# Performance work log

Measured on AMD Instinct MI355X. Metric: run time of the kernel, lower is better.

Reference implementation:

```python
import jax, jax.numpy as jnp
import numpy as np

EMBED_DIM = 768
NUM_HEADS = 12
HEAD_DIM = EMBED_DIM // NUM_HEADS


def setup_inputs() -> dict:
    key = jax.random.key(0)
    ks = jax.random.split(key, 9)
    B, N, D = 1, 4096, EMBED_DIM
    s = 1.0 / np.sqrt(D)
    x = jax.random.normal(ks[0], (B, N, D), dtype=jnp.float32)
    Wq = jax.random.normal(ks[1], (D, D), dtype=jnp.float32) * s
    Wk = jax.random.normal(ks[2], (D, D), dtype=jnp.float32) * s
    Wv = jax.random.normal(ks[3], (D, D), dtype=jnp.float32) * s
    Wo = jax.random.normal(ks[4], (D, D), dtype=jnp.float32) * s
    bq = jax.random.normal(ks[5], (D,), dtype=jnp.float32) * 0.01
    bk = jax.random.normal(ks[6], (D,), dtype=jnp.float32) * 0.01
    bv = jax.random.normal(ks[7], (D,), dtype=jnp.float32) * 0.01
    bo = jax.random.normal(ks[8], (D,), dtype=jnp.float32) * 0.01
    return {"x": x, "Wq": Wq, "bq": bq, "Wk": Wk, "bk": bk,
            "Wv": Wv, "bv": bv, "Wo": Wo, "bo": bo}


def reference(x, Wq, bq, Wk, bk, Wv, bv, Wo, bo):
    B, N, D = x.shape
    h, d = NUM_HEADS, HEAD_DIM
    # projections; torch Linear computes x @ W.T + b, here W is stored as (in, out)
    q = (x @ Wq + bq).reshape(B, N, h, d).transpose(0, 2, 1, 3)  # [B,h,N,d]
    k = (x @ Wk + bk).reshape(B, N, h, d).transpose(0, 2, 1, 3)
    v = (x @ Wv + bv).reshape(B, N, h, d).transpose(0, 2, 1, 3)
    scores = jnp.einsum('bhnd,bhmd->bhnm', q, k) / np.sqrt(d)  # [B,h,N,N]
    attn = jax.nn.softmax(scores, axis=-1)
    out = jnp.einsum('bhnm,bhmd->bhnd', attn, v)  # [B,h,N,d]
    out = out.transpose(0, 2, 1, 3).reshape(B, N, D)
    return out @ Wo + bo
```

## Files before the change

### kernel.cpp

```cpp
#include <hip/hip_runtime.h>
#include <stdint.h>

#define EMBED 768
#define NTOK 4096
#define NHEAD 12
#define HD 64

typedef __attribute__((ext_vector_type(8))) short bf16x8;
typedef __attribute__((ext_vector_type(4))) float f32x4;
typedef __attribute__((ext_vector_type(16))) float f32x16;
typedef unsigned short ushort_t;

#define QSCALE 0.18033688011112042f

__device__ __forceinline__ unsigned short f2bf(float f) {
  union { float f; unsigned u; } c; c.f = f;
  unsigned u = c.u;
  u += 0x7fffu + ((u >> 16) & 1u);
  return (unsigned short)(u >> 16);
}

__device__ __forceinline__ void gld16(const void* g, void* l) {
  __builtin_amdgcn_global_load_lds((const __attribute__((address_space(1))) void*)g,
                                   (__attribute__((address_space(3))) void*)l,
                                   16, 0, 0);
}

__global__ void cvt_x_kernel(const float* __restrict__ x, ushort_t* __restrict__ xb) {
  size_t i = ((size_t)blockIdx.x * 256 + threadIdx.x) * 8;
  float4 a = *(const float4*)(x + i);
  float4 b = *(const float4*)(x + i + 4);
  uint4 p;
  p.x = (unsigned)f2bf(a.x) | ((unsigned)f2bf(a.y) << 16);
  p.y = (unsigned)f2bf(a.z) | ((unsigned)f2bf(a.w) << 16);
  p.z = (unsigned)f2bf(b.x) | ((unsigned)f2bf(b.y) << 16);
  p.w = (unsigned)f2bf(b.z) | ((unsigned)f2bf(b.w) << 16);
  *(uint4*)(xb + i) = p;
}

__global__ void transpose_w4_kernel(const float* __restrict__ w0, const float* __restrict__ w1,
                                    const float* __restrict__ w2, const float* __restrict__ w3,
                                    ushort_t* __restrict__ d0, ushort_t* __restrict__ d1,
                                    ushort_t* __restrict__ d2, ushort_t* __restrict__ d3) {
  __shared__ float t[32][33];
  int z = blockIdx.z;
  const float* w = (z == 0) ? w0 : (z == 1) ? w1 : (z == 2) ? w2 : w3;
  ushort_t* wt   = (z == 0) ? d0 : (z == 1) ? d1 : (z == 2) ? d2 : d3;
  int bx = blockIdx.x * 32, by = blockIdx.y * 32;
  int tx = threadIdx.x, ty = threadIdx.y;
  #pragma unroll
  for (int i = 0; i < 32; i += 8)
    t[ty + i][tx] = w[(size_t)(by + ty + i) * EMBED + bx + tx];
  __syncthreads();
  #pragma unroll
  for (int i = 0; i < 32; i += 8)
    wt[(size_t)(bx + ty + i) * EMBED + by + tx] = f2bf(t[tx][ty + i]);
}

template<int MODE>
__global__ __launch_bounds__(256)
void gemm_bt_kernel(const ushort_t* __restrict__ A, const ushort_t* __restrict__ Bt,
                    const float* __restrict__ b0, const float* __restrict__ b1,
                    const float* __restrict__ b2,
                    ushort_t* __restrict__ qo, ushort_t* __restrict__ ko,
                    ushort_t* __restrict__ vto, float* __restrict__ out) {
  __shared__ ushort_t As[128 * 32];
  __shared__ ushort_t Bs[128 * 32];
  const int K = EMBED;
  int tid = threadIdx.x, lane = tid & 63, wid = tid >> 6;
  int wy = wid >> 1, wx = wid & 1;
  int r0 = lane >> 4, cq = lane & 15;
  int brow = blockIdx.y * 128, bcol = blockIdx.x * 128;

  f32x4 acc[4][4] = {};

  for (int k0 = 0; k0 < K; k0 += 32) {
    #pragma unroll
    for (int c = 0; c < 2; ++c) {
      int chunk = wid * 2 + c;
      int eoff = chunk * 512;
      int le = eoff + lane * 8;
      int row = le >> 5, col = le & 31;
      gld16(A + (size_t)(brow + row) * K + k0 + col, As + eoff);
      gld16(Bt + (size_t)(bcol + row) * K + k0 + col, Bs + eoff);
    }
    __syncthreads();
    bf16x8 af[4], bfr[4];
    #pragma unroll
    for (int i = 0; i < 4; ++i)
      af[i] = *(const bf16x8*)(As + (wy * 64 + i * 16 + cq) * 32 + r0 * 8);
    #pragma unroll
    for (int i = 0; i < 4; ++i)
      bfr[i] = *(const bf16x8*)(Bs + (wx * 64 + i * 16 + cq) * 32 + r0 * 8);
    #pragma unroll
    for (int i = 0; i < 4; ++i)
      #pragma unroll
      for (int j = 0; j < 4; ++j)
        acc[i][j] = __builtin_amdgcn_mfma_f32_16x16x32_bf16(af[i], bfr[j], acc[i][j], 0, 0, 0);
    __syncthreads();
  }

  int sec = bcol / 768;
  int ncol0 = bcol - sec * 768;
  const float* bias = (sec == 0) ? b0 : (sec == 1) ? b1 : b2;
  #pragma unroll
  for (int i = 0; i < 4; ++i) {
    #pragma unroll
    for (int j = 0; j < 4; ++j) {
      #pragma unroll
      for (int jj = 0; jj < 4; ++jj) {
        int m = brow + wy * 64 + i * 16 + r0 * 4 + jj;
        int nn = ncol0 + wx * 64 + j * 16 + cq;
        float val = acc[i][j][jj] + bias[nn];
        if constexpr (MODE == 0) {
          int head = nn >> 6, dd = nn & 63;
          if (sec == 0)       qo[((size_t)head * NTOK + m) * HD + dd] = f2bf(val * QSCALE);
          else if (sec == 1)  ko[((size_t)head * NTOK + m) * HD + dd] = f2bf(val);
          else                vto[((size_t)head * HD + dd) * NTOK + m] = f2bf(val);
        } else {
          out[(size_t)m * EMBED + nn] = val;
        }
      }
    }
  }
}

__device__ __forceinline__ void stage32(const ushort_t* kh, const ushort_t* vh,
                                        int kb, char* buf, int lane) {
  const int srow = lane >> 3, l7 = lane & 7;
  const int ksl = l7 ^ srow;
  const ushort_t* kg = kh + (size_t)kb * HD;
  #pragma unroll
  for (int i = 0; i < 4; ++i)
    gld16(kg + ((i * 8 + srow) * HD + ksl * 8), buf + i * 1024);
  char* vbuf = buf + 4096;
  const int srw = lane >> 2;
  const int vsl = (lane & 3) ^ (srw & 3);
  const ushort_t* vg = vh + kb;
  #pragma unroll
  for (int i = 0; i < 4; ++i)
    gld16(vg + ((size_t)(i * 16 + srw) * NTOK + vsl * 8), vbuf + i * 1024);
}

__global__ __launch_bounds__(256, 2)
void flash_kernel(const ushort_t* __restrict__ q, const ushort_t* __restrict__ k,
                  const ushort_t* __restrict__ vt, ushort_t* __restrict__ o) {
  __shared__ __align__(16) char lds[65536];
  const int tid = threadIdx.x;
  const int lane = tid & 63;
  const int ks = tid >> 6;
  const int head = blockIdx.y;
  const int qbase = blockIdx.x * 64;
  const int c31 = lane & 31;
  const int hi = lane >> 5;

  const ushort_t* qh = q + (size_t)head * NTOK * HD;
  const ushort_t* kh = k + (size_t)head * NTOK * HD;
  const ushort_t* vh = vt + (size_t)head * HD * NTOK;

  char* mybase = lds + ks * 16384;

  bf16x8 qf[2][4];
  #pragma unroll
  for (int qt = 0; qt < 2; ++qt)
    #pragma unroll
    for (int dc = 0; dc < 4; ++dc)
      qf[qt][dc] = *(const bf16x8*)(qh + (size_t)(qbase + qt * 32 + c31) * HD + dc * 16 + hi * 8);

  f32x16 oacc[2][2] = {};
  float lsum[2] = {0.f, 0.f};

  stage32(kh, vh, ks * 32, mybase, lane);

  #pragma unroll 2
  for (int it = 0; it < 32; ++it) {
    const int cur = it & 1;
    if (it < 31) {
      stage32(kh, vh, (ks + 4 * (it + 1)) * 32, mybase + (cur ^ 1) * 8192, lane);
      asm volatile("s_waitcnt vmcnt(8)" ::: "memory");
    } else {
      asm volatile("s_waitcnt vmcnt(0)" ::: "memory");
    }
    const char* kbuf = mybase + cur * 8192;
    const char* vbuf = kbuf + 4096;

    f32x16 s[2] = {};
    __builtin_amdgcn_s_setprio(1);
    #pragma unroll
    for (int dc = 0; dc < 4; ++dc) {
      bf16x8 kf = *(const bf16x8*)(kbuf + c31 * 128 + (((dc * 2 + hi) ^ (c31 & 7)) * 16));
      #pragma unroll
      for (int qt = 0; qt < 2; ++qt)
        s[qt] = __builtin_amdgcn_mfma_f32_32x32x16_bf16(kf, qf[qt][dc], s[qt], 0, 0, 0);
    }
    __builtin_amdgcn_s_setprio(0);

    union pfu { unsigned u[4]; bf16x8 v; };
    pfu pf[2][2];
    #pragma unroll
    for (int qt = 0; qt < 2; ++qt) {
      float p[16];
      #pragma unroll
      for (int r = 0; r < 16; ++r)
        p[r] = __builtin_amdgcn_exp2f(s[qt][r]);
      float s4[4];
      #pragma unroll
      for (int g = 0; g < 4; ++g)
        s4[g] = (p[4 * g] + p[4 * g + 1]) + (p[4 * g + 2] + p[4 * g + 3]);
      lsum[qt] += (s4[0] + s4[1]) + (s4[2] + s4[3]);
      unsigned w[8];
      #pragma unroll
      for (int m = 0; m < 8; ++m)
        asm("v_cvt_pk_bf16_f32 %0, %1, %2" : "=v"(w[m]) : "v"(p[2 * m]), "v"(p[2 * m + 1]));
      #pragma unroll
      for (int kc = 0; kc < 2; ++kc) {
        #pragma unroll
        for (int e = 0; e < 2; ++e) {
          unsigned a = w[e + 4 * kc];
          unsigned b = w[e + 4 * kc + 2];
          asm("v_permlane32_swap_b32 %0, %1" : "+v"(a), "+v"(b));
          pf[qt][kc].u[e] = a;
          pf[qt][kc].u[e + 2] = b;
        }
      }
    }

    __builtin_amdgcn_s_setprio(1);
    #pragma unroll
    for (int kc = 0; kc < 2; ++kc)
      #pragma unroll
      for (int dt = 0; dt < 2; ++dt) {
        bf16x8 vf = *(const bf16x8*)(vbuf + (dt * 32 + c31) * 64 + (((kc * 2 + hi) ^ (c31 & 3)) * 16));
        #pragma unroll
        for (int qt = 0; qt < 2; ++qt)
          oacc[dt][qt] = __builtin_amdgcn_mfma_f32_32x32x16_bf16(vf, pf[qt][kc].v, oacc[dt][qt], 0, 0, 0);
      }
    __builtin_amdgcn_s_setprio(0);
  }

  __syncthreads();
  float* Oacc = (float*)lds;
  float* lacc = Oacc + 64 * 68;
  for (int t = tid; t < 64 * 68 + 64; t += 256)
    ((float*)lds)[t] = 0.f;
  __syncthreads();
  #pragma unroll
  for (int qt = 0; qt < 2; ++qt) {
    int qq = qt * 32 + c31;
    atomicAdd(&lacc[qq], lsum[qt]);
    #pragma unroll
    for (int dt = 0; dt < 2; ++dt)
      #pragma unroll
      for (int g = 0; g < 4; ++g) {
        int dd = dt * 32 + 8 * g + 4 * hi;
        #pragma unroll
        for (int j = 0; j < 4; ++j)
          atomicAdd(&Oacc[qq * 68 + dd + j], oacc[dt][qt][4 * g + j]);
      }
  }
  __syncthreads();

  int qq = tid >> 2, seg = tid & 3;
  float linv = 1.0f / lacc[qq];
  unsigned outw[8];
  #pragma unroll
  for (int m = 0; m < 8; ++m) {
    float lo = Oacc[qq * 68 + seg * 16 + 2 * m] * linv;
    float hh = Oacc[qq * 68 + seg * 16 + 2 * m + 1] * linv;
    asm("v_cvt_pk_bf16_f32 %0, %1, %2" : "=v"(outw[m]) : "v"(lo), "v"(hh));
  }
  ushort_t* op = o + (size_t)(qbase + qq) * EMBED + head * HD + seg * 16;
  uint4 u0; u0.x = outw[0]; u0.y = outw[1]; u0.z = outw[2]; u0.w = outw[3];
  uint4 u1; u1.x = outw[4]; u1.y = outw[5]; u1.z = outw[6]; u1.w = outw[7];
  *(uint4*)op = u0;
  *((uint4*)op + 1) = u1;
}

extern "C" void kernel_launch(void* const* d_in, const int* in_sizes, int n_in,
                              void* d_out, int out_size, void* d_ws, size_t ws_size,
                              hipStream_t stream) {
  const float* x  = (const float*)d_in[0];
  const float* Wq = (const float*)d_in[1];
  const float* bq = (const float*)d_in[2];
  const float* Wk = (const float*)d_in[3];
  const float* bk = (const float*)d_in[4];
  const float* Wv = (const float*)d_in[5];
  const float* bv = (const float*)d_in[6];
  const float* Wo = (const float*)d_in[7];
  const float* bo = (const float*)d_in[8];
  float* out = (float*)d_out;

  char* ws = (char*)d_ws;
  ushort_t* xb    = (ushort_t*)ws;  ws += (size_t)NTOK * EMBED * 2;
  ushort_t* wqkvt = (ushort_t*)ws;  ws += (size_t)3 * EMBED * EMBED * 2;
  ushort_t* wot   = (ushort_t*)ws;  ws += (size_t)EMBED * EMBED * 2;
  ushort_t* qb    = (ushort_t*)ws;  ws += (size_t)NTOK * EMBED * 2;
  ushort_t* kb2   = (ushort_t*)ws;  ws += (size_t)NTOK * EMBED * 2;
  ushort_t* vtb   = (ushort_t*)ws;  ws += (size_t)NTOK * EMBED * 2;
  ushort_t* ao    = (ushort_t*)ws;  ws += (size_t)NTOK * EMBED * 2;

  cvt_x_kernel<<<(NTOK * EMBED) / (256 * 8), 256, 0, stream>>>(x, xb);
  transpose_w4_kernel<<<dim3(24, 24, 4), dim3(32, 8), 0, stream>>>(
      Wq, Wk, Wv, Wo,
      wqkvt, wqkvt + (size_t)EMBED * EMBED, wqkvt + (size_t)2 * EMBED * EMBED, wot);

  gemm_bt_kernel<0><<<dim3(2304 / 128, NTOK / 128), 256, 0, stream>>>(
      xb, wqkvt, bq, bk, bv, qb, kb2, vtb, nullptr);

  flash_kernel<<<dim3(NTOK / 64, NHEAD), 256, 0, stream>>>(qb, kb2, vtb, ao);

  gemm_bt_kernel<1><<<dim3(EMBED / 128, NTOK / 128), 256, 0, stream>>>(
      ao, wot, bo, nullptr, nullptr, nullptr, nullptr, nullptr, out);
}
```

Measured before the change: 265.0 us.

## Write V row-major, transpose with padded stride, remap flash blocks across XCDs

```diff
diff --git a/kernel.cpp b/kernel.cpp
--- a/kernel.cpp
+++ b/kernel.cpp
@@ -5,6 +5,7 @@
 #define NTOK 4096
 #define NHEAD 12
 #define HD 64
+#define VSTRIDE 4128
 
 typedef __attribute__((ext_vector_type(8))) short bf16x8;
 typedef __attribute__((ext_vector_type(4))) float f32x4;
@@ -57,13 +58,30 @@
     wt[(size_t)(bx + ty + i) * EMBED + by + tx] = f2bf(t[tx][ty + i]);
 }
 
+__global__ void transpose_v_kernel(const ushort_t* __restrict__ vb, ushort_t* __restrict__ vt) {
+  __shared__ ushort_t t[32][33];
+  int head = blockIdx.z;
+  int bx = blockIdx.x * 32;
+  int by = blockIdx.y * 32;
+  int tx = threadIdx.x, ty = threadIdx.y;
+  const ushort_t* src = vb + (size_t)head * NTOK * HD;
+  ushort_t* dst = vt + (size_t)head * HD * VSTRIDE;
+  #pragma unroll
+  for (int i = 0; i < 32; i += 8)
+    t[ty + i][tx] = src[(size_t)(by + ty + i) * HD + bx + tx];
+  __syncthreads();
+  #pragma unroll
+  for (int i = 0; i < 32; i += 8)
+    dst[(size_t)(bx + ty + i) * VSTRIDE + by + tx] = t[tx][ty + i];
+}
+
 template<int MODE>
 __global__ __launch_bounds__(256)
 void gemm_bt_kernel(const ushort_t* __restrict__ A, const ushort_t* __restrict__ Bt,
                     const float* __restrict__ b0, const float* __restrict__ b1,
                     const float* __restrict__ b2,
                     ushort_t* __restrict__ qo, ushort_t* __restrict__ ko,
-                    ushort_t* __restrict__ vto, float* __restrict__ out) {
+                    ushort_t* __restrict__ vbo, float* __restrict__ out) {
   __shared__ ushort_t As[128 * 32];
   __shared__ ushort_t Bs[128 * 32];
   const int K = EMBED;
@@ -116,7 +134,7 @@
           int head = nn >> 6, dd = nn & 63;
           if (sec == 0)       qo[((size_t)head * NTOK + m) * HD + dd] = f2bf(val * QSCALE);
           else if (sec == 1)  ko[((size_t)head * NTOK + m) * HD + dd] = f2bf(val);
-          else                vto[((size_t)head * HD + dd) * NTOK + m] = f2bf(val);
+          else                vbo[((size_t)head * NTOK + m) * HD + dd] = f2bf(val);
         } else {
           out[(size_t)m * EMBED + nn] = val;
         }
@@ -139,7 +157,7 @@
   const ushort_t* vg = vh + kb;
   #pragma unroll
   for (int i = 0; i < 4; ++i)
-    gld16(vg + ((size_t)(i * 16 + srw) * NTOK + vsl * 8), vbuf + i * 1024);
+    gld16(vg + ((size_t)(i * 16 + srw) * VSTRIDE + vsl * 8), vbuf + i * 1024);
 }
 
 __global__ __launch_bounds__(256, 2)
@@ -149,14 +167,16 @@
   const int tid = threadIdx.x;
   const int lane = tid & 63;
   const int ks = tid >> 6;
-  const int head = blockIdx.y;
-  const int qbase = blockIdx.x * 64;
+  const int b = blockIdx.x;
+  const int slot = (b & 7) * 96 + (b >> 3);
+  const int head = slot >> 6;
+  const int qbase = (slot & 63) * 64;
   const int c31 = lane & 31;
   const int hi = lane >> 5;
 
   const ushort_t* qh = q + (size_t)head * NTOK * HD;
   const ushort_t* kh = k + (size_t)head * NTOK * HD;
-  const ushort_t* vh = vt + (size_t)head * HD * NTOK;
+  const ushort_t* vh = vt + (size_t)head * HD * VSTRIDE;
 
   char* mybase = lds + ks * 16384;
 
@@ -217,10 +237,10 @@
         #pragma unroll
         for (int e = 0; e < 2; ++e) {
           unsigned a = w[e + 4 * kc];
-          unsigned b = w[e + 4 * kc + 2];
-          asm("v_permlane32_swap_b32 %0, %1" : "+v"(a), "+v"(b));
+          unsigned b2 = w[e + 4 * kc + 2];
+          asm("v_permlane32_swap_b32 %0, %1" : "+v"(a), "+v"(b2));
           pf[qt][kc].u[e] = a;
-          pf[qt][kc].u[e + 2] = b;
+          pf[qt][kc].u[e + 2] = b2;
         }
       }
     }
@@ -296,8 +316,9 @@
   ushort_t* wot   = (ushort_t*)ws;  ws += (size_t)EMBED * EMBED * 2;
   ushort_t* qb    = (ushort_t*)ws;  ws += (size_t)NTOK * EMBED * 2;
   ushort_t* kb2   = (ushort_t*)ws;  ws += (size_t)NTOK * EMBED * 2;
-  ushort_t* vtb   = (ushort_t*)ws;  ws += (size_t)NTOK * EMBED * 2;
+  ushort_t* vtb   = (ushort_t*)ws;  ws += (size_t)NHEAD * HD * VSTRIDE * 2;
   ushort_t* ao    = (ushort_t*)ws;  ws += (size_t)NTOK * EMBED * 2;
+  ushort_t* vb    = ao;
 
   cvt_x_kernel<<<(NTOK * EMBED) / (256 * 8), 256, 0, stream>>>(x, xb);
   transpose_w4_kernel<<<dim3(24, 24, 4), dim3(32, 8), 0, stream>>>(
@@ -305,9 +326,11 @@
       wqkvt, wqkvt + (size_t)EMBED * EMBED, wqkvt + (size_t)2 * EMBED * EMBED, wot);
 
   gemm_bt_kernel<0><<<dim3(2304 / 128, NTOK / 128), 256, 0, stream>>>(
-      xb, wqkvt, bq, bk, bv, qb, kb2, vtb, nullptr);
-
-  flash_kernel<<<dim3(NTOK / 64, NHEAD), 256, 0, stream>>>(qb, kb2, vtb, ao);
+      xb, wqkvt, bq, bk, bv, qb, kb2, vb, nullptr);
+
+  transpose_v_kernel<<<dim3(2, 128, NHEAD), dim3(32, 8), 0, stream>>>(vb, vtb);
+
+  flash_kernel<<<dim3(NTOK / 64 * NHEAD), 256, 0, stream>>>(qb, kb2, vtb, ao);
 
   gemm_bt_kernel<1><<<dim3(EMBED / 128, NTOK / 128), 256, 0, stream>>>(
       ao, wot, bo, nullptr, nullptr, nullptr, nullptr, nullptr, out);
```

Result: no change. 260.4 us (-1.7%).
